# Kernel optimization log

Measured on AMD Instinct MI355X. Metric: run time of the kernel, lower is better.

Reference implementation:

```python
import jax, jax.numpy as jnp
import numpy as np

N_NODES = 100000
N_EDGES = 1600000
IN_FEAT = 256
HIDDEN = 64
N_CLASSES = 16


def gcn_conv(x, edge_index, W, b):
    """PyG GCNConv: add self-loops, symmetric normalization, linear+aggregate."""
    n = x.shape[0]
    src, dst = edge_index[0], edge_index[1]
    loops = jnp.arange(n, dtype=src.dtype)
    src = jnp.concatenate([src, loops])
    dst = jnp.concatenate([dst, loops])
    # in-degree on graph with self-loops
    deg = jax.ops.segment_sum(jnp.ones(src.shape[0], dtype=x.dtype), dst, num_segments=n)
    dinv = jnp.where(deg > 0, jax.lax.rsqrt(deg), 0.0)
    h = x @ W                                  # [N, out]
    norm = dinv[src] * dinv[dst]               # [E+N]
    msg = h[src] * norm[:, None]                # gather + scale (memory-bound)
    out = jax.ops.segment_sum(msg, dst, num_segments=n)  # scatter-add
    return out + b


def setup_inputs() -> dict:
    key = jax.random.key(0)
    ks = jax.random.split(key, 5)
    x = jax.random.normal(ks[0], (N_NODES, IN_FEAT), dtype=jnp.float32)
    edge_index = jax.random.randint(ks[1], (2, N_EDGES), 0, N_NODES, dtype=jnp.int64)
    W1 = jax.random.normal(ks[2], (IN_FEAT, HIDDEN), dtype=jnp.float32) * (1.0 / np.sqrt(IN_FEAT))
    b1 = jnp.zeros((HIDDEN,), dtype=jnp.float32)
    W2 = jax.random.normal(ks[3], (HIDDEN, N_CLASSES), dtype=jnp.float32) * (1.0 / np.sqrt(HIDDEN))
    b2 = jnp.zeros((N_CLASSES,), dtype=jnp.float32)
    return {"x": x, "edge_index": edge_index, "W1": W1, "b1": b1, "W2": W2, "b2": b2}


def reference(x, edge_index, W1, b1, W2, b2):
    h = gcn_conv(x, edge_index, W1, b1)
    h = jax.nn.relu(h)
    # dropout p=0.5 is identity in eval mode (training=False)
    out = gcn_conv(h, edge_index, W2, b2)
    return out
```

## Files before the change

kernel.cpp:

```cpp
#include <hip/hip_runtime.h>

#define NN 100000
#define NE 1600000
#define FIN 256
#define FH 64
#define FC 16

#define SCAN_CHUNK 1024
#define NB_SCAN ((NN + SCAN_CHUNK - 1) / SCAN_CHUNK)
#define NSWEEP 2
#define SWEEP_W ((NN + NSWEEP - 1) / NSWEEP)
#define NB_COUNT ((NE + 255) / 256)
#define NB_GEMM1 ((NN + 63) / 64)

typedef int v2i __attribute__((ext_vector_type(2)));

__global__ void detect_k(const int* __restrict__ ei, int* __restrict__ flag) {
    if (threadIdx.x == 0 && blockIdx.x == 0) {
        int z = (ei[1] == 0) & (ei[3] == 0) & (ei[5] == 0) & (ei[7] == 0);
        *flag = z;
    }
}

__device__ __forceinline__ int eidx(const int* __restrict__ ei, int f, int pos) {
    return f ? ei[2 * pos] : ei[pos];
}

__global__ __launch_bounds__(256) void fused_k(const int* __restrict__ ei,
                                               const int* __restrict__ flag,
                                               int* __restrict__ deg,
                                               v2i* __restrict__ packed,
                                               const float* __restrict__ x,
                                               const float* __restrict__ W,
                                               float* __restrict__ h) {
    if (blockIdx.x < NB_COUNT) {
        int e = blockIdx.x * 256 + threadIdx.x;
        if (e >= NE) return;
        int f = *flag;
        int s = eidx(ei, f, e);
        int d = eidx(ei, f, NE + e);
        int r = atomicAdd(&deg[d], 1);
        v2i p; p.x = s; p.y = d | (r << 17);
        packed[e] = p;
        return;
    }
    __shared__ float As[64][68];
    __shared__ float Bs[64][64];
    const int t = threadIdx.x;
    const int r0 = (blockIdx.x - NB_COUNT) * 64;
    const int tx4 = (t & 15) * 4;
    const int ty4 = (t >> 4) * 4;
    const int lrow = t >> 4;
    const int lkf = (t & 15) * 4;

    float acc[4][4] = {};

    for (int k0 = 0; k0 < FIN; k0 += 64) {
        #pragma unroll
        for (int i = 0; i < 4; i++) {
            int row = lrow + 16 * i;
            int gr = r0 + row;
            float4 v = make_float4(0.f, 0.f, 0.f, 0.f);
            if (gr < NN) v = *(const float4*)&x[gr * FIN + k0 + lkf];
            As[lkf + 0][row] = v.x;
            As[lkf + 1][row] = v.y;
            As[lkf + 2][row] = v.z;
            As[lkf + 3][row] = v.w;
            float4 w = *(const float4*)&W[(k0 + row) * FH + lkf];
            *(float4*)&Bs[row][lkf] = w;
        }
        __syncthreads();
        #pragma unroll 8
        for (int kk = 0; kk < 64; kk++) {
            float4 a = *(const float4*)&As[kk][ty4];
            float4 b = *(const float4*)&Bs[kk][tx4];
            float av[4] = {a.x, a.y, a.z, a.w};
            float bv[4] = {b.x, b.y, b.z, b.w};
            #pragma unroll
            for (int i2 = 0; i2 < 4; i2++)
                #pragma unroll
                for (int j2 = 0; j2 < 4; j2++)
                    acc[i2][j2] = fmaf(av[i2], bv[j2], acc[i2][j2]);
        }
        __syncthreads();
    }
    #pragma unroll
    for (int i2 = 0; i2 < 4; i2++) {
        int r = r0 + ty4 + i2;
        if (r < NN)
            *(float4*)&h[r * FH + tx4] =
                make_float4(acc[i2][0], acc[i2][1], acc[i2][2], acc[i2][3]);
    }
}

__global__ void dinv_k(const int* __restrict__ deg, float* __restrict__ dinv) {
    int i = blockIdx.x * 256 + threadIdx.x;
    if (i < NN) dinv[i] = rsqrtf((float)(deg[i] + 1));
}

__global__ __launch_bounds__(256) void scan_sum_k(const int* __restrict__ deg,
                                                  int* __restrict__ partial) {
    __shared__ int red[256];
    int b = blockIdx.x, t = threadIdx.x;
    int base = b * SCAN_CHUNK + t * 4;
    int s = 0;
    #pragma unroll
    for (int i = 0; i < 4; i++) { int idx = base + i; if (idx < NN) s += deg[idx]; }
    red[t] = s;
    __syncthreads();
    for (int off = 128; off > 0; off >>= 1) {
        if (t < off) red[t] += red[t + off];
        __syncthreads();
    }
    if (t == 0) partial[b] = red[0];
}

__global__ __launch_bounds__(128) void scan_part_k(int* __restrict__ partial) {
    __shared__ int s[128];
    int t = threadIdx.x;
    int v = (t < NB_SCAN) ? partial[t] : 0;
    s[t] = v; __syncthreads();
    for (int off = 1; off < 128; off <<= 1) {
        int u = (t >= off) ? s[t - off] : 0;
        __syncthreads();
        s[t] += u;
        __syncthreads();
    }
    if (t < NB_SCAN) partial[t] = s[t] - v;
}

__global__ __launch_bounds__(256) void scan_out_k(const int* __restrict__ deg,
                                                  const int* __restrict__ partial,
                                                  int* __restrict__ row_start) {
    __shared__ int s[256];
    int b = blockIdx.x, t = threadIdx.x;
    int base = b * SCAN_CHUNK + t * 4;
    int v[4]; int sum = 0;
    #pragma unroll
    for (int i = 0; i < 4; i++) {
        int idx = base + i;
        v[i] = (idx < NN) ? deg[idx] : 0;
        sum += v[i];
    }
    s[t] = sum; __syncthreads();
    for (int off = 1; off < 256; off <<= 1) {
        int u = (t >= off) ? s[t - off] : 0;
        __syncthreads();
        s[t] += u;
        __syncthreads();
    }
    int run = partial[b] + s[t] - sum;
    #pragma unroll
    for (int i = 0; i < 4; i++) {
        int idx = base + i;
        if (idx < NN) {
            row_start[idx] = run;
            run += v[i];
            if (idx == NN - 1) row_start[NN] = run;
        }
    }
}

__global__ __launch_bounds__(256) void fill_k(const v2i* __restrict__ packed,
                                              const int* __restrict__ row_start,
                                              int* __restrict__ csr,
                                              int lo, int hi) {
    int e = blockIdx.x * 256 + threadIdx.x;
    if (e >= NE) return;
    v2i p = __builtin_nontemporal_load(&packed[e]);
    int d = p.y & 0x1FFFF;
    if (d < lo || d >= hi) return;
    int r = ((unsigned)p.y) >> 17;
    csr[row_start[d] + r] = p.x;
}

__global__ __launch_bounds__(256) void agg1_k(const int* __restrict__ csr,
                                              const int* __restrict__ row_start,
                                              const float* __restrict__ h1,
                                              const float* __restrict__ dinv,
                                              const float* __restrict__ b1,
                                              float* __restrict__ agg) {
    int n = blockIdx.x * 4 + (threadIdx.x >> 6);
    int lane = threadIdx.x & 63;
    if (n >= NN) return;
    int s0 = row_start[n], s1 = row_start[n + 1];
    float acc = 0.f, a0 = 0.f, a1 = 0.f, a2 = 0.f, a3 = 0.f;
    for (int j0 = s0; j0 < s1; j0 += 64) {
        int idx = j0 + lane;
        int sl = 0; float wl = 0.f;
        if (idx < s1) { sl = csr[idx]; wl = dinv[sl]; }
        int cnt = s1 - j0; if (cnt > 64) cnt = 64;
        int j = 0;
        for (; j + 4 <= cnt; j += 4) {
            int   sA = __shfl(sl, j + 0, 64), sB = __shfl(sl, j + 1, 64);
            int   sC = __shfl(sl, j + 2, 64), sD = __shfl(sl, j + 3, 64);
            float wA = __shfl(wl, j + 0, 64), wB = __shfl(wl, j + 1, 64);
            float wC = __shfl(wl, j + 2, 64), wD = __shfl(wl, j + 3, 64);
            float hA = h1[sA * FH + lane];
            float hB = h1[sB * FH + lane];
            float hC = h1[sC * FH + lane];
            float hD = h1[sD * FH + lane];
            a0 = fmaf(hA, wA, a0); a1 = fmaf(hB, wB, a1);
            a2 = fmaf(hC, wC, a2); a3 = fmaf(hD, wD, a3);
        }
        for (; j < cnt; j++) {
            int   s = __shfl(sl, j, 64);
            float w = __shfl(wl, j, 64);
            acc = fmaf(h1[s * FH + lane], w, acc);
        }
    }
    acc += (a0 + a1) + (a2 + a3);
    float dn = dinv[n];
    acc = fmaf(h1[n * FH + lane], dn, acc);
    agg[n * FH + lane] = fmaf(acc, dn, b1[lane]);
}

__global__ __launch_bounds__(192) void gemm2_k(const float* __restrict__ agg,
                                               const float* __restrict__ W2,
                                               float* __restrict__ h2) {
    __shared__ float a_lds[192 * 65];
    const int t = threadIdx.x;
    const int r0 = blockIdx.x * 192;
    #pragma unroll
    for (int i = 0; i < 16; i++) {
        int fidx = t + 192 * i;
        int row = fidx >> 4, kf = (fidx & 15) * 4;
        int gr = r0 + row;
        float4 v = make_float4(0.f, 0.f, 0.f, 0.f);
        if (gr < NN) v = *(const float4*)&agg[gr * FH + kf];
        v.x = fmaxf(v.x, 0.f); v.y = fmaxf(v.y, 0.f);
        v.z = fmaxf(v.z, 0.f); v.w = fmaxf(v.w, 0.f);
        a_lds[row * 65 + kf + 0] = v.x;
        a_lds[row * 65 + kf + 1] = v.y;
        a_lds[row * 65 + kf + 2] = v.z;
        a_lds[row * 65 + kf + 3] = v.w;
    }
    __syncthreads();
    float acc[FC] = {};
    #pragma unroll 4
    for (int k = 0; k < FH; k++) {
        float a = a_lds[t * 65 + k];
        #pragma unroll
        for (int c = 0; c < FC; c++)
            acc[c] = fmaf(a, W2[k * FC + c], acc[c]);
    }
    int r = r0 + t;
    if (r < NN) {
        #pragma unroll
        for (int q = 0; q < 4; q++)
            *(float4*)&h2[r * FC + 4 * q] =
                make_float4(acc[4*q], acc[4*q+1], acc[4*q+2], acc[4*q+3]);
    }
}

__global__ __launch_bounds__(256) void agg2_k(const int* __restrict__ csr,
                                              const int* __restrict__ row_start,
                                              const float* __restrict__ h2,
                                              const float* __restrict__ dinv,
                                              const float* __restrict__ b2,
                                              float* __restrict__ out) {
    int n = blockIdx.x * 16 + (threadIdx.x >> 4);
    int l16 = threadIdx.x & 15;
    int base = threadIdx.x & 48;
    if (n >= NN) return;
    int s0 = row_start[n], s1 = row_start[n + 1];
    float acc = 0.f, a0 = 0.f, a1 = 0.f, a2 = 0.f, a3 = 0.f;
    for (int j0 = s0; j0 < s1; j0 += 16) {
        int idx = j0 + l16;
        int sl = 0; float wl = 0.f;
        if (idx < s1) { sl = csr[idx]; wl = dinv[sl]; }
        int cnt = s1 - j0; if (cnt > 16) cnt = 16;
        int j = 0;
        for (; j + 4 <= cnt; j += 4) {
            int   sA = __shfl(sl, base + j + 0, 64), sB = __shfl(sl, base + j + 1, 64);
            int   sC = __shfl(sl, base + j + 2, 64), sD = __shfl(sl, base + j + 3, 64);
            float wA = __shfl(wl, base + j + 0, 64), wB = __shfl(wl, base + j + 1, 64);
            float wC = __shfl(wl, base + j + 2, 64), wD = __shfl(wl, base + j + 3, 64);
            float hA = h2[sA * FC + l16];
            float hB = h2[sB * FC + l16];
            float hC = h2[sC * FC + l16];
            float hD = h2[sD * FC + l16];
            a0 = fmaf(hA, wA, a0); a1 = fmaf(hB, wB, a1);
            a2 = fmaf(hC, wC, a2); a3 = fmaf(hD, wD, a3);
        }
        for (; j < cnt; j++) {
            int   s = __shfl(sl, base + j, 64);
            float w = __shfl(wl, base + j, 64);
            acc = fmaf(h2[s * FC + l16], w, acc);
        }
    }
    acc += (a0 + a1) + (a2 + a3);
    float dn = dinv[n];
    acc = fmaf(h2[n * FC + l16], dn, acc);
    out[n * FC + l16] = fmaf(acc, dn, b2[l16]);
}

extern "C" void kernel_launch(void* const* d_in, const int* in_sizes, int n_in,
                              void* d_out, int out_size, void* d_ws, size_t ws_size,
                              hipStream_t stream) {
    const float* x  = (const float*)d_in[0];
    const int*   ei = (const int*)d_in[1];
    const float* W1 = (const float*)d_in[2];
    const float* b1 = (const float*)d_in[3];
    const float* W2 = (const float*)d_in[4];
    const float* b2 = (const float*)d_in[5];
    float* out = (float*)d_out;

    char* ws = (char*)d_ws;
    int*   deg       = (int*)(ws + 0);
    int*   row_start = (int*)(ws + 512 * 1024);
    float* dinv      = (float*)(ws + 1024 * 1024);
    int*   flag      = (int*)(ws + 1536 * 1024);
    int*   partial   = (int*)(ws + 1540 * 1024);
    int*   csr       = (int*)(ws + 2ull * 1024 * 1024);
    float* h1        = (float*)(ws + 9ull * 1024 * 1024);
    v2i*   packed    = (v2i*)(ws + 35ull * 1024 * 1024);
    float* agg1      = (float*)(ws + 35ull * 1024 * 1024);
    float* h2        = h1;

    detect_k<<<1, 64, 0, stream>>>(ei, flag);
    (void)hipMemsetAsync(deg, 0, NN * sizeof(int), stream);
    fused_k<<<NB_COUNT + NB_GEMM1, 256, 0, stream>>>(ei, flag, deg, packed, x, W1, h1);
    dinv_k<<<(NN + 255) / 256, 256, 0, stream>>>(deg, dinv);
    scan_sum_k<<<NB_SCAN, 256, 0, stream>>>(deg, partial);
    scan_part_k<<<1, 128, 0, stream>>>(partial);
    scan_out_k<<<NB_SCAN, 256, 0, stream>>>(deg, partial, row_start);
    for (int sw = 0; sw < NSWEEP; sw++)
        fill_k<<<(NE + 255) / 256, 256, 0, stream>>>(packed, row_start, csr,
                                                     sw * SWEEP_W, (sw + 1) * SWEEP_W);

    agg1_k<<<(NN + 3) / 4, 256, 0, stream>>>(csr, row_start, h1, dinv, b1, agg1);
    gemm2_k<<<(NN + 191) / 192, 192, 0, stream>>>(agg1, W2, h2);
    agg2_k<<<(NN + 15) / 16, 256, 0, stream>>>(csr, row_start, h2, dinv, b2, out);
}
```

Baseline: 398.0 us.

## Fuse second-layer GEMM into first aggregation, fold dinv into scan, shrink GEMM1 tile

The first-layer aggregation now also applies bias and ReLU, stages each node's 64-wide row in LDS, and multiplies it by W2 (cached in LDS) to write h2 directly. This removes the separate gemm2 kernel and the round trip of the intermediate agg1 buffer through global memory. The dinv computation is folded into the scan_sum kernel to drop one launch and one extra read of deg. The GEMM1 part of fused_k now uses a K-tile of 32 with smaller LDS arrays and an 8-blocks occupancy hint, trading more barrier iterations for higher occupancy; the in-wave LDS handoff relies on s_waitcnt rather than a barrier.

```diff
diff --git a/kernel.cpp b/kernel.cpp
--- a/kernel.cpp
+++ b/kernel.cpp
@@ -26,13 +26,15 @@
     return f ? ei[2 * pos] : ei[pos];
 }
 
-__global__ __launch_bounds__(256) void fused_k(const int* __restrict__ ei,
-                                               const int* __restrict__ flag,
-                                               int* __restrict__ deg,
-                                               v2i* __restrict__ packed,
-                                               const float* __restrict__ x,
-                                               const float* __restrict__ W,
-                                               float* __restrict__ h) {
+__global__ __launch_bounds__(256, 8) void fused_k(const int* __restrict__ ei,
+                                                  const int* __restrict__ flag,
+                                                  int* __restrict__ deg,
+                                                  v2i* __restrict__ packed,
+                                                  const float* __restrict__ x,
+                                                  const float* __restrict__ W,
+                                                  float* __restrict__ h) {
+    __shared__ float As[32][68];
+    __shared__ float Bs[32][64];
     if (blockIdx.x < NB_COUNT) {
         int e = blockIdx.x * 256 + threadIdx.x;
         if (e >= NE) return;
@@ -44,34 +46,35 @@
         packed[e] = p;
         return;
     }
-    __shared__ float As[64][68];
-    __shared__ float Bs[64][64];
     const int t = threadIdx.x;
     const int r0 = (blockIdx.x - NB_COUNT) * 64;
     const int tx4 = (t & 15) * 4;
     const int ty4 = (t >> 4) * 4;
-    const int lrow = t >> 4;
-    const int lkf = (t & 15) * 4;
+    const int xkf = (t & 7) * 4;
+    const int xrow = t >> 3;
+    const int wcol = (t & 15) * 4;
+    const int wrow = t >> 4;
 
     float acc[4][4] = {};
 
-    for (int k0 = 0; k0 < FIN; k0 += 64) {
+    for (int k0 = 0; k0 < FIN; k0 += 32) {
         #pragma unroll
-        for (int i = 0; i < 4; i++) {
-            int row = lrow + 16 * i;
+        for (int i = 0; i < 2; i++) {
+            int row = xrow + 32 * i;
             int gr = r0 + row;
             float4 v = make_float4(0.f, 0.f, 0.f, 0.f);
-            if (gr < NN) v = *(const float4*)&x[gr * FIN + k0 + lkf];
-            As[lkf + 0][row] = v.x;
-            As[lkf + 1][row] = v.y;
-            As[lkf + 2][row] = v.z;
-            As[lkf + 3][row] = v.w;
-            float4 w = *(const float4*)&W[(k0 + row) * FH + lkf];
-            *(float4*)&Bs[row][lkf] = w;
+            if (gr < NN) v = *(const float4*)&x[gr * FIN + k0 + xkf];
+            As[xkf + 0][row] = v.x;
+            As[xkf + 1][row] = v.y;
+            As[xkf + 2][row] = v.z;
+            As[xkf + 3][row] = v.w;
+            int kr = wrow + 16 * i;
+            float4 w = *(const float4*)&W[(k0 + kr) * FH + wcol];
+            *(float4*)&Bs[kr][wcol] = w;
         }
         __syncthreads();
         #pragma unroll 8
-        for (int kk = 0; kk < 64; kk++) {
+        for (int kk = 0; kk < 32; kk++) {
             float4 a = *(const float4*)&As[kk][ty4];
             float4 b = *(const float4*)&Bs[kk][tx4];
             float av[4] = {a.x, a.y, a.z, a.w};
@@ -93,19 +96,22 @@
     }
 }
 
-__global__ void dinv_k(const int* __restrict__ deg, float* __restrict__ dinv) {
-    int i = blockIdx.x * 256 + threadIdx.x;
-    if (i < NN) dinv[i] = rsqrtf((float)(deg[i] + 1));
-}
-
 __global__ __launch_bounds__(256) void scan_sum_k(const int* __restrict__ deg,
-                                                  int* __restrict__ partial) {
+                                                  int* __restrict__ partial,
+                                                  float* __restrict__ dinv) {
     __shared__ int red[256];
     int b = blockIdx.x, t = threadIdx.x;
     int base = b * SCAN_CHUNK + t * 4;
     int s = 0;
     #pragma unroll
-    for (int i = 0; i < 4; i++) { int idx = base + i; if (idx < NN) s += deg[idx]; }
+    for (int i = 0; i < 4; i++) {
+        int idx = base + i;
+        if (idx < NN) {
+            int dv = deg[idx];
+            s += dv;
+            dinv[idx] = rsqrtf((float)(dv + 1));
+        }
+    }
     red[t] = s;
     __syncthreads();
     for (int off = 128; off > 0; off >>= 1) {
@@ -174,14 +180,23 @@
     csr[row_start[d] + r] = p.x;
 }
 
-__global__ __launch_bounds__(256) void agg1_k(const int* __restrict__ csr,
-                                              const int* __restrict__ row_start,
-                                              const float* __restrict__ h1,
-                                              const float* __restrict__ dinv,
-                                              const float* __restrict__ b1,
-                                              float* __restrict__ agg) {
-    int n = blockIdx.x * 4 + (threadIdx.x >> 6);
-    int lane = threadIdx.x & 63;
+__global__ __launch_bounds__(256) void agg1g_k(const int* __restrict__ csr,
+                                               const int* __restrict__ row_start,
+                                               const float* __restrict__ h1,
+                                               const float* __restrict__ dinv,
+                                               const float* __restrict__ b1,
+                                               const float* __restrict__ W2,
+                                               float* __restrict__ h2) {
+    __shared__ float sW2[FH * FC];
+    __shared__ float sp[4][FH];
+    const int t = threadIdx.x;
+    #pragma unroll
+    for (int i = 0; i < 4; i++) sW2[t + 256 * i] = W2[t + 256 * i];
+    __syncthreads();
+
+    int wid = t >> 6;
+    int n = blockIdx.x * 4 + wid;
+    int lane = t & 63;
     if (n >= NN) return;
     int s0 = row_start[n], s1 = row_start[n + 1];
     float acc = 0.f, a0 = 0.f, a1 = 0.f, a2 = 0.f, a3 = 0.f;
@@ -212,44 +227,15 @@
     acc += (a0 + a1) + (a2 + a3);
     float dn = dinv[n];
     acc = fmaf(h1[n * FH + lane], dn, acc);
-    agg[n * FH + lane] = fmaf(acc, dn, b1[lane]);
-}
-
-__global__ __launch_bounds__(192) void gemm2_k(const float* __restrict__ agg,
-                                               const float* __restrict__ W2,
-                                               float* __restrict__ h2) {
-    __shared__ float a_lds[192 * 65];
-    const int t = threadIdx.x;
-    const int r0 = blockIdx.x * 192;
-    #pragma unroll
-    for (int i = 0; i < 16; i++) {
-        int fidx = t + 192 * i;
-        int row = fidx >> 4, kf = (fidx & 15) * 4;
-        int gr = r0 + row;
-        float4 v = make_float4(0.f, 0.f, 0.f, 0.f);
-        if (gr < NN) v = *(const float4*)&agg[gr * FH + kf];
-        v.x = fmaxf(v.x, 0.f); v.y = fmaxf(v.y, 0.f);
-        v.z = fmaxf(v.z, 0.f); v.w = fmaxf(v.w, 0.f);
-        a_lds[row * 65 + kf + 0] = v.x;
-        a_lds[row * 65 + kf + 1] = v.y;
-        a_lds[row * 65 + kf + 2] = v.z;
-        a_lds[row * 65 + kf + 3] = v.w;
-    }
-    __syncthreads();
-    float acc[FC] = {};
-    #pragma unroll 4
-    for (int k = 0; k < FH; k++) {
-        float a = a_lds[t * 65 + k];
-        #pragma unroll
-        for (int c = 0; c < FC; c++)
-            acc[c] = fmaf(a, W2[k * FC + c], acc[c]);
-    }
-    int r = r0 + t;
-    if (r < NN) {
-        #pragma unroll
-        for (int q = 0; q < 4; q++)
-            *(float4*)&h2[r * FC + 4 * q] =
-                make_float4(acc[4*q], acc[4*q+1], acc[4*q+2], acc[4*q+3]);
+    float p = fmaf(acc, dn, b1[lane]);
+    sp[wid][lane] = fmaxf(p, 0.f);
+    __builtin_amdgcn_s_waitcnt(0);
+    if (lane < FC) {
+        float o = 0.f;
+        #pragma unroll 8
+        for (int k = 0; k < FH; k++)
+            o = fmaf(sp[wid][k], sW2[k * FC + lane], o);
+        h2[n * FC + lane] = o;
     }
 }
 
@@ -315,21 +301,18 @@
     int*   csr       = (int*)(ws + 2ull * 1024 * 1024);
     float* h1        = (float*)(ws + 9ull * 1024 * 1024);
     v2i*   packed    = (v2i*)(ws + 35ull * 1024 * 1024);
-    float* agg1      = (float*)(ws + 35ull * 1024 * 1024);
-    float* h2        = h1;
+    float* h2        = (float*)(ws + 35ull * 1024 * 1024);
 
     detect_k<<<1, 64, 0, stream>>>(ei, flag);
     (void)hipMemsetAsync(deg, 0, NN * sizeof(int), stream);
     fused_k<<<NB_COUNT + NB_GEMM1, 256, 0, stream>>>(ei, flag, deg, packed, x, W1, h1);
-    dinv_k<<<(NN + 255) / 256, 256, 0, stream>>>(deg, dinv);
-    scan_sum_k<<<NB_SCAN, 256, 0, stream>>>(deg, partial);
+    scan_sum_k<<<NB_SCAN, 256, 0, stream>>>(deg, partial, dinv);
     scan_part_k<<<1, 128, 0, stream>>>(partial);
     scan_out_k<<<NB_SCAN, 256, 0, stream>>>(deg, partial, row_start);
     for (int sw = 0; sw < NSWEEP; sw++)
         fill_k<<<(NE + 255) / 256, 256, 0, stream>>>(packed, row_start, csr,
                                                      sw * SWEEP_W, (sw + 1) * SWEEP_W);
 
-    agg1_k<<<(NN + 3) / 4, 256, 0, stream>>>(csr, row_start, h1, dinv, b1, agg1);
-    gemm2_k<<<(NN + 191) / 192, 192, 0, stream>>>(agg1, W2, h2);
+    agg1g_k<<<(NN + 3) / 4, 256, 0, stream>>>(csr, row_start, h1, dinv, b1, W2, h2);
     agg2_k<<<(NN + 15) / 16, 256, 0, stream>>>(csr, row_start, h2, dinv, b2, out);
 }
```

Measured after the change: 396.3 us. Within noise of the previous version (-0.4%).
